# Optimization experiments

Hardware: AMD Instinct MI355X
Metric: run time of the kernel (lower is better)

## Reference

```python
import jax, jax.numpy as jnp
import numpy as np

N_RAYS = 65536
N_SAMPLES = 2_097_152
HID = 64
L_PTS, L_DIR = 10, 4
STEP = 5e-3
WHITE_BKGD = True


def posenc(x, L):
    # x [..., 3] -> [..., 3 + 6L]
    freqs = (2.0 ** jnp.arange(L)).astype(x.dtype)            # [L]
    ang = x[..., None, :] * freqs[:, None]                     # [..., L, 3]
    enc = jnp.concatenate([jnp.sin(ang), jnp.cos(ang)], -1)   # [..., L, 6]
    return jnp.concatenate([x, enc.reshape(x.shape[:-1] + (6 * L,))], -1)


def setup_inputs() -> dict:
    key = jax.random.key(0)
    ks = jax.random.split(key, 12)
    rays_o = jax.random.normal(ks[0], (N_RAYS, 3), jnp.float32)
    viewdirs = jax.random.normal(ks[1], (N_RAYS, 3), jnp.float32)
    viewdirs = viewdirs / jnp.linalg.norm(viewdirs, axis=-1, keepdims=True)
    ray_indices = jnp.sort(jax.random.randint(ks[2], (N_SAMPLES,), 0, N_RAYS, jnp.int32))
    t_starts = jax.random.uniform(ks[3], (N_SAMPLES,), jnp.float32, 0.0, 4.0)
    t_ends = t_starts + STEP

    def w(k, shape):
        return jax.random.normal(k, shape, jnp.float32) / jnp.sqrt(shape[0])

    D_PTS = 3 + 6 * L_PTS   # 63
    D_DIR = 3 + 6 * L_DIR   # 27
    return dict(
        rays_o=rays_o, viewdirs=viewdirs, t_starts=t_starts, t_ends=t_ends,
        W1=w(ks[4], (D_PTS, HID)), b1=jnp.zeros((HID,), jnp.float32),
        W2=w(ks[5], (HID, HID)), b2=jnp.zeros((HID,), jnp.float32),
        Wd=w(ks[6], (HID, 1)), bd=jnp.zeros((1,), jnp.float32),
        Wf=w(ks[7], (HID, HID)), bf=jnp.zeros((HID,), jnp.float32),
        Wr1=w(ks[8], (HID + D_DIR, HID)), br1=jnp.zeros((HID,), jnp.float32),
        Wr2=w(ks[9], (HID, 3)), br2=jnp.zeros((3,), jnp.float32),
        ray_indices=ray_indices,
    )


def reference(rays_o, viewdirs, t_starts, t_ends,
              W1, b1, W2, b2, Wd, bd, Wf, bf, Wr1, br1, Wr2, br2,
              ray_indices):
    t_mid = 0.5 * (t_starts + t_ends)                     # [S]
    o = rays_o[ray_indices]                               # gather [S,3]
    d = viewdirs[ray_indices]                             # gather [S,3]
    pts = o + d * t_mid[:, None]                          # [S,3]

    # small NeRF MLP (self.net): sigma + view-dependent rgb
    h = jax.nn.relu(posenc(pts, L_PTS) @ W1 + b1)
    h = jax.nn.relu(h @ W2 + b2)
    sigma = jax.nn.relu((h @ Wd + bd)[:, 0])              # relu(density)
    feat = h @ Wf + bf
    hd = jax.nn.relu(jnp.concatenate([feat, posenc(d, L_DIR)], -1) @ Wr1 + br1)
    rgb = jax.nn.sigmoid(hd @ Wr2 + br2)                  # [S,3]

    alpha = 1.0 - jnp.exp(-sigma * (t_ends - t_starts))   # [S], in [0,1)

    # per-ray exclusive transmittance via segment exclusive cumsum in log space
    log1m = jnp.log1p(-jnp.clip(alpha, 0.0, 1.0 - 1e-7))  # <= 0
    excl = jnp.cumsum(log1m) - log1m                      # global exclusive cumsum
    counts = jax.ops.segment_sum(jnp.ones_like(ray_indices), ray_indices, N_RAYS)
    start_idx = jnp.cumsum(counts) - counts               # first sample of each ray
    offset = jnp.where(counts > 0, excl[jnp.clip(start_idx, 0, N_SAMPLES - 1)], 0.0)
    T = jnp.exp(excl - offset[ray_indices])               # transmittance [S]
    w = T * alpha                                         # render weights [S]

    colors = jax.ops.segment_sum(w[:, None] * rgb, ray_indices, N_RAYS)   # [R,3]
    opac = jax.ops.segment_sum(w, ray_indices, N_RAYS)                    # [R]
    depth = jax.ops.segment_sum(w * t_mid, ray_indices, N_RAYS)           # [R]

    bkgd = 1.0 if WHITE_BKGD else 0.0
    colors = colors + (1.0 - opac)[:, None] * bkgd
    return colors, opac[:, None], depth[:, None]
```

## Files before the change

kernel.cpp:

```cpp
#include <hip/hip_runtime.h>
#include <math.h>

#define NR 65536
#define NS 2097152

typedef __attribute__((ext_vector_type(4))) float f32x4;
typedef __attribute__((ext_vector_type(2))) float f32x2;
typedef __attribute__((ext_vector_type(8))) short short8;



__device__ __forceinline__ uint packbf(float a, float b) {
    __bf16 lo = (__bf16)a, hi = (__bf16)b;
    ushort ul = __builtin_bit_cast(ushort, lo);
    ushort uh = __builtin_bit_cast(ushort, hi);
    return (uint)ul | ((uint)uh << 16);
}
__device__ __forceinline__ float bflo(uint u) { return __builtin_bit_cast(float, u << 16); }

__global__ void setup_kernel(const float* __restrict__ viewdirs,
                             uint4* __restrict__ dtab,
                             int* __restrict__ start, int* __restrict__ end,
                             const float* __restrict__ W1, const float* __restrict__ W2,
                             const float* __restrict__ Wf, const float* __restrict__ Wr1,
                             const float* __restrict__ Wd, const float* __restrict__ Wr2,
                             uint4* __restrict__ wfrag) {
    int b = blockIdx.x, tid = threadIdx.x;
    if (b < 256) {
        int r = b * 256 + tid;
        float dx = viewdirs[3 * r + 0], dy = viewdirs[3 * r + 1], dz = viewdirs[3 * r + 2];
        float de[32];
        de[0] = dx; de[1] = dy; de[2] = dz;
        float sx = __sinf(dx), cx = __cosf(dx);
        float sy = __sinf(dy), cy = __cosf(dy);
        float sz = __sinf(dz), cz = __cosf(dz);
        #pragma unroll
        for (int l = 0; l < 4; ++l) {
            de[3 + 6 * l + 0] = sx; de[3 + 6 * l + 1] = sy; de[3 + 6 * l + 2] = sz;
            de[3 + 6 * l + 3] = cx; de[3 + 6 * l + 4] = cy; de[3 + 6 * l + 5] = cz;
            float nsx = 2.0f * sx * cx, nsy = 2.0f * sy * cy, nsz = 2.0f * sz * cz;
            cx = fmaf(-2.0f * sx, sx, 1.0f);
            cy = fmaf(-2.0f * sy, sy, 1.0f);
            cz = fmaf(-2.0f * sz, sz, 1.0f);
            sx = nsx; sy = nsy; sz = nsz;
        }
        #pragma unroll
        for (int k = 27; k < 32; ++k) de[k] = 0.0f;
        #pragma unroll
        for (int c = 0; c < 4; ++c) {
            uint4 q = make_uint4(packbf(de[8 * c + 0], de[8 * c + 1]),
                                 packbf(de[8 * c + 2], de[8 * c + 3]),
                                 packbf(de[8 * c + 4], de[8 * c + 5]),
                                 packbf(de[8 * c + 6], de[8 * c + 7]));
            dtab[(size_t)r * 4 + c] = q;
        }
    } else if (b < 512) {
        int r = (b - 256) * 256 + tid;
        start[r] = 0; end[r] = 0;
    } else {
        int t = (b - 512) * 256 + tid;
        if (t >= 40 * 64) return;
        int f = t >> 6, lane = t & 63;
        int c = lane & 15;
        uint q[4];
        if (f < 36) {
            const float* W; int kmax, fl;
            if (f < 8)       { W = W1;  kmax = 63; fl = f; }
            else if (f < 16) { W = W2;  kmax = 64; fl = f - 8; }
            else if (f < 24) { W = Wf;  kmax = 64; fl = f - 16; }
            else             { W = Wr1; kmax = 91; fl = f - 24; }
            int ks = fl >> 2, ft = fl & 3;
            int n = ft * 16 + c;
            int kb = ks * 32 + ((lane >> 4) * 8);
            #pragma unroll
            for (int j = 0; j < 4; ++j) {
                int k0 = kb + 2 * j, k1 = k0 + 1;
                float v0 = (k0 < kmax) ? W[k0 * 64 + n] : 0.0f;
                float v1 = (k1 < kmax) ? W[k1 * 64 + n] : 0.0f;
                q[j] = packbf(v0, v1);
            }
        } else if (f < 38) {
            int kb = (f - 36) * 32 + ((lane >> 4) * 8);
            #pragma unroll
            for (int j = 0; j < 4; ++j) {
                float v0 = (c == 0) ? Wd[kb + 2 * j] : 0.0f;
                float v1 = (c == 0) ? Wd[kb + 2 * j + 1] : 0.0f;
                q[j] = packbf(v0, v1);
            }
        } else {
            int kb = (f - 38) * 32 + ((lane >> 4) * 8);
            #pragma unroll
            for (int j = 0; j < 4; ++j) {
                float v0 = (c < 3) ? Wr2[(kb + 2 * j) * 3 + c] : 0.0f;
                float v1 = (c < 3) ? Wr2[(kb + 2 * j + 1) * 3 + c] : 0.0f;
                q[j] = packbf(v0, v1);
            }
        }
        wfrag[(size_t)f * 64 + lane] = make_uint4(q[0], q[1], q[2], q[3]);
    }
}

template <int KS, bool RELU, bool SIGMA, bool DIRB>
__device__ __forceinline__ void dense_layer(uint* S, const uint4* __restrict__ wfrag,
                                            int fb, const float* __restrict__ bias,
                                            float bd0, const uint (&ro)[2],
                                            const uint (&wo)[4],
                                            int lane, const uint4 (&dirB)[4],
                                            float* sigout) {
    const int g = lane >> 4;
    uint4 wf[KS * 4];
    #pragma unroll
    for (int i = 0; i < KS * 4; ++i) wf[i] = wfrag[(size_t)(fb + i) * 64 + lane];
    uint4 wsg[2];
    if constexpr (SIGMA) {
        wsg[0] = wfrag[36 * 64 + lane];
        wsg[1] = wfrag[37 * 64 + lane];
    }
    float4 bfr[4];
    #pragma unroll
    for (int ft = 0; ft < 4; ++ft)
        bfr[ft] = *(const float4*)(bias + 16 * ft + 4 * g);

    #pragma unroll
    for (int st = 0; st < 4; ++st) {
        const uint stoff = (uint)st * 512u;
        uint4 B[KS];
        #pragma unroll
        for (int ks = 0; ks < KS; ++ks) {
            if (DIRB && ks == KS - 1) B[ks] = dirB[st];
            else B[ks] = *(const uint4*)&S[ro[ks] + stoff];
        }
        f32x4 acc[4];
        #pragma unroll
        for (int ft = 0; ft < 4; ++ft)
            acc[ft] = (f32x4){bfr[ft].x, bfr[ft].y, bfr[ft].z, bfr[ft].w};
        f32x4 sacc;
        if constexpr (SIGMA) sacc = (f32x4){(g == 0) ? bd0 : 0.0f, 0.0f, 0.0f, 0.0f};
        #pragma unroll
        for (int ks = 0; ks < KS; ++ks) {
            short8 bv = __builtin_bit_cast(short8, B[ks]);
            #pragma unroll
            for (int ft = 0; ft < 4; ++ft)
                acc[ft] = __builtin_amdgcn_mfma_f32_16x16x32_bf16(
                    __builtin_bit_cast(short8, wf[ks * 4 + ft]), bv, acc[ft], 0, 0, 0);
            if constexpr (SIGMA)
                sacc = __builtin_amdgcn_mfma_f32_16x16x32_bf16(
                    __builtin_bit_cast(short8, wsg[ks]), bv, sacc, 0, 0, 0);
        }
        #pragma unroll
        for (int ft = 0; ft < 4; ++ft) {
            f32x2 lo = {acc[ft][0], acc[ft][1]};
            f32x2 hi = {acc[ft][2], acc[ft][3]};
            if constexpr (RELU) {
                lo = __builtin_elementwise_max(lo, (f32x2){0.0f, 0.0f});
                hi = __builtin_elementwise_max(hi, (f32x2){0.0f, 0.0f});
            }
            uint2 v = make_uint2(packbf(lo.x, lo.y), packbf(hi.x, hi.y));
            *(uint2*)&S[wo[ft] + stoff] = v;
        }
        if constexpr (SIGMA) sigout[st] = sacc[0];
    }
}

__global__ __launch_bounds__(256, 4) void fused_mlp(
    const float* __restrict__ rays_o, const float* __restrict__ viewdirs,
    const float* __restrict__ t_starts, const float* __restrict__ t_ends,
    const float* __restrict__ b1, const float* __restrict__ b2,
    const float* __restrict__ bd, const float* __restrict__ bf_,
    const float* __restrict__ br1, const float* __restrict__ br2,
    const int* __restrict__ ridx, const uint4* __restrict__ wfrag,
    const uint4* __restrict__ dtab, uint2* __restrict__ rgba,
    float* __restrict__ tmarr, int* __restrict__ start, int* __restrict__ end)
{
    __shared__ uint S[8192];

    const int tid = threadIdx.x;
    const int w = tid >> 6, lane = tid & 63;
    const int g = lane >> 4, s = lane & 15;
    const uint sm = (uint)(s & 7);
    const uint wgb = (uint)w * 2048u;
    const uint rowb = wgb + (uint)s * 32u;
    const int sb0 = blockIdx.x * 256 + w * 64;

    int ridx4[4];
    #pragma unroll
    for (int st = 0; st < 4; ++st) ridx4[st] = ridx[sb0 + st * 16 + s];
    uint4 dirB[4];
    #pragma unroll
    for (int st = 0; st < 4; ++st) dirB[st] = dtab[(size_t)ridx4[st] * 4 + g];

    const int si = sb0 + g * 16 + s;
    const int rr = ridx4[g];

    {
        int r_prev = ridx[(si == 0) ? 0 : si - 1];
        int r_next = ridx[(si == NS - 1) ? NS - 1 : si + 1];
        if (si == 0 || r_prev != rr) start[rr] = si;
        if (si == NS - 1 || r_next != rr) end[rr] = si + 1;
    }

    float ts = t_starts[si], te = t_ends[si];
    float tm = 0.5f * (ts + te), dtv = te - ts;
    float dx = viewdirs[3 * rr + 0], dy = viewdirs[3 * rr + 1], dz = viewdirs[3 * rr + 2];
    float px = rays_o[3 * rr + 0] + dx * tm;
    float py = rays_o[3 * rr + 1] + dy * tm;
    float pz = rays_o[3 * rr + 2] + dz * tm;
    tmarr[si] = tm;

    const uint ownbase = wgb + (uint)g * 512u + (uint)s * 32u;
    uint ro[2], wo[4];
    #pragma unroll
    for (int ks = 0; ks < 2; ++ks)
        ro[ks] = rowb + 4u * (((uint)(g + 4 * ks)) ^ sm);
    #pragma unroll
    for (int ft = 0; ft < 4; ++ft)
        wo[ft] = rowb + 4u * (((uint)(2 * ft + (g >> 1))) ^ sm) + 2u * (uint)(g & 1);

    {
        float enc[64];
        enc[0] = px; enc[1] = py; enc[2] = pz;
        f32x2 sxy = {__sinf(px), __sinf(py)};
        f32x2 cxy = {__cosf(px), __cosf(py)};
        float sz = __sinf(pz), cz = __cosf(pz);
        #pragma unroll
        for (int l = 0; l < 10; ++l) {
            enc[3 + 6 * l + 0] = sxy.x; enc[3 + 6 * l + 1] = sxy.y; enc[3 + 6 * l + 2] = sz;
            enc[3 + 6 * l + 3] = cxy.x; enc[3 + 6 * l + 4] = cxy.y; enc[3 + 6 * l + 5] = cz;
            f32x2 nsxy = 2.0f * sxy * cxy;
            cxy = 1.0f - 2.0f * sxy * sxy;
            float nsz = 2.0f * sz * cz;
            cz = fmaf(-2.0f * sz, sz, 1.0f);
            sxy = nsxy; sz = nsz;
        }
        enc[63] = 0.0f;
        #pragma unroll
        for (int ch = 0; ch < 8; ++ch) {
            uint4 q = make_uint4(packbf(enc[8 * ch + 0], enc[8 * ch + 1]),
                                 packbf(enc[8 * ch + 2], enc[8 * ch + 3]),
                                 packbf(enc[8 * ch + 4], enc[8 * ch + 5]),
                                 packbf(enc[8 * ch + 6], enc[8 * ch + 7]));
            *(uint4*)&S[ownbase + 4u * (((uint)ch) ^ sm)] = q;
        }
    }

    float sig4[4];
    float bd0 = bd[0];
    uint4 dummy[4];

    dense_layer<2, true,  false, false>(S, wfrag,  0, b1,  0.0f, ro, wo, lane, dummy, sig4);
    dense_layer<2, true,  false, false>(S, wfrag,  8, b2,  0.0f, ro, wo, lane, dummy, sig4);
    dense_layer<2, false, true,  false>(S, wfrag, 16, bf_, bd0,  ro, wo, lane, dummy, sig4);
    dense_layer<3, true,  false, true >(S, wfrag, 24, br1, 0.0f, ro, wo, lane, dirB, sig4);

    {
        uint4 wr0 = wfrag[38 * 64 + lane], wr1f = wfrag[39 * 64 + lane];
        float c0 = br2[0], c1 = br2[1], c2 = br2[2];
        #pragma unroll
        for (int st = 0; st < 4; ++st) {
            const uint stoff = (uint)st * 512u;
            uint4 B0 = *(const uint4*)&S[ro[0] + stoff];
            uint4 B1 = *(const uint4*)&S[ro[1] + stoff];
            f32x4 acc = (g == 0) ? (f32x4){c0, c1, c2, 0.0f}
                                 : (f32x4){0.0f, 0.0f, 0.0f, 0.0f};
            acc = __builtin_amdgcn_mfma_f32_16x16x32_bf16(
                __builtin_bit_cast(short8, wr0), __builtin_bit_cast(short8, B0), acc, 0, 0, 0);
            acc = __builtin_amdgcn_mfma_f32_16x16x32_bf16(
                __builtin_bit_cast(short8, wr1f), __builtin_bit_cast(short8, B1), acc, 0, 0, 0);
            float dte = __shfl(dtv, st * 16 + (lane & 15));
            if (lane < 16) {
                float sg = fmaxf(sig4[st], 0.0f);
                float alpha = 1.0f - __expf(-sg * dte);
                float r0 = 1.0f / (1.0f + __expf(-acc[0]));
                float r1 = 1.0f / (1.0f + __expf(-acc[1]));
                float r2 = 1.0f / (1.0f + __expf(-acc[2]));
                uint2 o;
                o.x = packbf(r0, r1);
                o.y = packbf(r2, alpha);
                rgba[sb0 + st * 16 + lane] = o;
            }
        }
    }
}

__global__ void render_kernel(const uint2* __restrict__ rgba,
                              const float* __restrict__ tmarr,
                              const int* __restrict__ start,
                              const int* __restrict__ end,
                              float* __restrict__ out)
{
    int r = blockIdx.x * blockDim.x + threadIdx.x;
    if (r >= NR) return;
    int sb = start[r], e = end[r];
    float T = 1.0f, c0 = 0.0f, c1 = 0.0f, c2 = 0.0f, op = 0.0f, dp = 0.0f;
    for (int i = sb; i < e; ++i) {
        uint2 q = rgba[i];
        float tmid = tmarr[i];
        float vr = bflo(q.x & 0xffffu), vg = bflo(q.x >> 16);
        float vb = bflo(q.y & 0xffffu), va = bflo(q.y >> 16);
        float wgt = T * va;
        c0 += wgt * vr; c1 += wgt * vg; c2 += wgt * vb;
        op += wgt; dp += wgt * tmid;
        T *= (1.0f - va);
    }
    float bg = 1.0f - op;
    c0 += bg; c1 += bg; c2 += bg;
    out[3 * r + 0] = c0;
    out[3 * r + 1] = c1;
    out[3 * r + 2] = c2;
    out[3 * NR + r] = op;
    out[4 * NR + r] = dp;
}

extern "C" void kernel_launch(void* const* d_in, const int* in_sizes, int n_in,
                              void* d_out, int out_size, void* d_ws, size_t ws_size,
                              hipStream_t stream) {
    const float* rays_o   = (const float*)d_in[0];
    const float* viewdirs = (const float*)d_in[1];
    const float* t_starts = (const float*)d_in[2];
    const float* t_ends   = (const float*)d_in[3];
    const float* W1  = (const float*)d_in[4];
    const float* b1  = (const float*)d_in[5];
    const float* W2  = (const float*)d_in[6];
    const float* b2  = (const float*)d_in[7];
    const float* Wd  = (const float*)d_in[8];
    const float* bd  = (const float*)d_in[9];
    const float* Wf  = (const float*)d_in[10];
    const float* bf_ = (const float*)d_in[11];
    const float* Wr1 = (const float*)d_in[12];
    const float* br1 = (const float*)d_in[13];
    const float* Wr2 = (const float*)d_in[14];
    const float* br2 = (const float*)d_in[15];
    const int* ridx  = (const int*)d_in[16];
    float* out = (float*)d_out;

    char* ws = (char*)d_ws;
    uint2* rgba  = (uint2*)ws;
    float* tmarr = (float*)(ws + (size_t)NS * 8);
    int* start   = (int*)(ws + (size_t)NS * 12);
    int* end     = start + NR;
    uint4* wfrag = (uint4*)(ws + (size_t)NS * 12 + (size_t)NR * 8);
    uint4* dtab  = (uint4*)(ws + (size_t)NS * 12 + (size_t)NR * 8 + 40 * 64 * 16);

    setup_kernel<<<522, 256, 0, stream>>>(viewdirs, dtab, start, end,
                                          W1, W2, Wf, Wr1, Wd, Wr2, wfrag);
    fused_mlp<<<NS / 256, 256, 0, stream>>>(
        rays_o, viewdirs, t_starts, t_ends,
        b1, b2, bd, bf_, br1, br2, ridx, wfrag, dtab, rgba, tmarr, start, end);
    render_kernel<<<NR / 256, 256, 0, stream>>>(rgba, tmarr, start, end, out);
}
```

Measured before the change: 143.0 us.

## Double-buffer MLP weight fragments in registers and prefetch next layer

Weight fragments for each dense layer are now loaded into one of two register buffers one layer ahead, so global loads for layer k+1 overlap the MFMA work of layer k. The first two layers' weights are loaded at kernel start, before the gathers and positional encoding. Launch bounds drop from 4 to 3 blocks per SM to leave room for the extra 24 uint4 registers per thread, which lowers occupancy and latency hiding from other waves.

```diff
diff --git a/kernel.cpp b/kernel.cpp
--- a/kernel.cpp
+++ b/kernel.cpp
@@ -100,22 +100,21 @@
     }
 }
 
+template <int N>
+__device__ __forceinline__ void loadf(uint4* dst, const uint4* __restrict__ wfrag,
+                                      int fb, int lane) {
+    #pragma unroll
+    for (int i = 0; i < N; ++i) dst[i] = wfrag[(size_t)(fb + i) * 64 + lane];
+}
+
 template <int KS, bool RELU, bool SIGMA, bool DIRB>
-__device__ __forceinline__ void dense_layer(uint* S, const uint4* __restrict__ wfrag,
-                                            int fb, const float* __restrict__ bias,
+__device__ __forceinline__ void dense_layer(uint* S, const uint4 (&wf)[12],
+                                            const float* __restrict__ bias,
                                             float bd0, const uint (&ro)[2],
                                             const uint (&wo)[4],
                                             int lane, const uint4 (&dirB)[4],
                                             float* sigout) {
     const int g = lane >> 4;
-    uint4 wf[KS * 4];
-    #pragma unroll
-    for (int i = 0; i < KS * 4; ++i) wf[i] = wfrag[(size_t)(fb + i) * 64 + lane];
-    uint4 wsg[2];
-    if constexpr (SIGMA) {
-        wsg[0] = wfrag[36 * 64 + lane];
-        wsg[1] = wfrag[37 * 64 + lane];
-    }
     float4 bfr[4];
     #pragma unroll
     for (int ft = 0; ft < 4; ++ft)
@@ -145,7 +144,7 @@
                     __builtin_bit_cast(short8, wf[ks * 4 + ft]), bv, acc[ft], 0, 0, 0);
             if constexpr (SIGMA)
                 sacc = __builtin_amdgcn_mfma_f32_16x16x32_bf16(
-                    __builtin_bit_cast(short8, wsg[ks]), bv, sacc, 0, 0, 0);
+                    __builtin_bit_cast(short8, wf[8 + ks]), bv, sacc, 0, 0, 0);
         }
         #pragma unroll
         for (int ft = 0; ft < 4; ++ft) {
@@ -162,7 +161,7 @@
     }
 }
 
-__global__ __launch_bounds__(256, 4) void fused_mlp(
+__global__ __launch_bounds__(256, 3) void fused_mlp(
     const float* __restrict__ rays_o, const float* __restrict__ viewdirs,
     const float* __restrict__ t_starts, const float* __restrict__ t_ends,
     const float* __restrict__ b1, const float* __restrict__ b2,
@@ -182,6 +181,10 @@
     const uint rowb = wgb + (uint)s * 32u;
     const int sb0 = blockIdx.x * 256 + w * 64;
 
+    uint4 wfA[12], wfB[12];
+    loadf<8>(wfA, wfrag, 0, lane);
+    loadf<8>(wfB, wfrag, 8, lane);
+
     int ridx4[4];
     #pragma unroll
     for (int st = 0; st < 4; ++st) ridx4[st] = ridx[sb0 + st * 16 + s];
@@ -247,13 +250,21 @@
     float bd0 = bd[0];
     uint4 dummy[4];
 
-    dense_layer<2, true,  false, false>(S, wfrag,  0, b1,  0.0f, ro, wo, lane, dummy, sig4);
-    dense_layer<2, true,  false, false>(S, wfrag,  8, b2,  0.0f, ro, wo, lane, dummy, sig4);
-    dense_layer<2, false, true,  false>(S, wfrag, 16, bf_, bd0,  ro, wo, lane, dummy, sig4);
-    dense_layer<3, true,  false, true >(S, wfrag, 24, br1, 0.0f, ro, wo, lane, dirB, sig4);
+    dense_layer<2, true,  false, false>(S, wfA, b1,  0.0f, ro, wo, lane, dummy, sig4);
+    loadf<8>(wfA, wfrag, 16, lane);
+    wfA[8] = wfrag[36 * 64 + lane];
+    wfA[9] = wfrag[37 * 64 + lane];
+
+    dense_layer<2, true,  false, false>(S, wfB, b2,  0.0f, ro, wo, lane, dummy, sig4);
+    loadf<12>(wfB, wfrag, 24, lane);
+
+    dense_layer<2, false, true,  false>(S, wfA, bf_, bd0,  ro, wo, lane, dummy, sig4);
+    uint4 wr0 = wfrag[38 * 64 + lane];
+    uint4 wr1f = wfrag[39 * 64 + lane];
+
+    dense_layer<3, true,  false, true >(S, wfB, br1, 0.0f, ro, wo, lane, dirB, sig4);
 
     {
-        uint4 wr0 = wfrag[38 * 64 + lane], wr1f = wfrag[39 * 64 + lane];
         float c0 = br2[0], c1 = br2[1], c2 = br2[2];
         #pragma unroll
         for (int st = 0; st < 4; ++st) {
```

Measured after the change: 156.5 us. +9.4%, slower.

## Fold linear feature layer into first rendering layer weights and bias

Applied to the files above, without the earlier changes.

Because the feature layer has no activation, its weight matrix is premultiplied into the first 64 rows of the rendering layer in the setup kernel, and the combined bias is precomputed. The fused MLP then runs one combined layer that also produces sigma, removing a full dense layer with its MFMAs and LDS round trip per sample. The precomputed product is rounded to bf16 once, which changes numerics slightly.

```diff
diff --git a/kernel.cpp b/kernel.cpp
--- a/kernel.cpp
+++ b/kernel.cpp
@@ -24,7 +24,8 @@
                              const float* __restrict__ W1, const float* __restrict__ W2,
                              const float* __restrict__ Wf, const float* __restrict__ Wr1,
                              const float* __restrict__ Wd, const float* __restrict__ Wr2,
-                             uint4* __restrict__ wfrag) {
+                             const float* __restrict__ bf_, const float* __restrict__ br1,
+                             uint4* __restrict__ wfrag, float* __restrict__ b34) {
     int b = blockIdx.x, tid = threadIdx.x;
     if (b < 256) {
         int r = b * 256 + tid;
@@ -57,21 +58,18 @@
     } else if (b < 512) {
         int r = (b - 256) * 256 + tid;
         start[r] = 0; end[r] = 0;
-    } else {
+    } else if (b < 520) {
         int t = (b - 512) * 256 + tid;
-        if (t >= 40 * 64) return;
         int f = t >> 6, lane = t & 63;
-        int c = lane & 15;
+        int c = lane & 15, g2 = lane >> 4;
         uint q[4];
-        if (f < 36) {
-            const float* W; int kmax, fl;
-            if (f < 8)       { W = W1;  kmax = 63; fl = f; }
-            else if (f < 16) { W = W2;  kmax = 64; fl = f - 8; }
-            else if (f < 24) { W = Wf;  kmax = 64; fl = f - 16; }
-            else             { W = Wr1; kmax = 91; fl = f - 24; }
+        if (f < 16) {
+            const float* W = (f < 8) ? W1 : W2;
+            int kmax = (f < 8) ? 63 : 64;
+            int fl = f & 7;
             int ks = fl >> 2, ft = fl & 3;
             int n = ft * 16 + c;
-            int kb = ks * 32 + ((lane >> 4) * 8);
+            int kb = ks * 32 + g2 * 8;
             #pragma unroll
             for (int j = 0; j < 4; ++j) {
                 int k0 = kb + 2 * j, k1 = k0 + 1;
@@ -79,8 +77,34 @@
                 float v1 = (k1 < kmax) ? W[k1 * 64 + n] : 0.0f;
                 q[j] = packbf(v0, v1);
             }
-        } else if (f < 38) {
-            int kb = (f - 36) * 32 + ((lane >> 4) * 8);
+        } else if (f < 24) {
+            int fl = f - 16;
+            int ks = fl >> 2, ft = fl & 3;
+            int m = ft * 16 + c;
+            int kb = ks * 32 + g2 * 8;
+            #pragma unroll
+            for (int j = 0; j < 4; ++j) {
+                int k0 = kb + 2 * j, k1 = k0 + 1;
+                float v0 = 0.0f, v1 = 0.0f;
+                for (int p = 0; p < 64; ++p) {
+                    float w = Wr1[p * 64 + m];
+                    v0 = fmaf(Wf[k0 * 64 + p], w, v0);
+                    v1 = fmaf(Wf[k1 * 64 + p], w, v1);
+                }
+                q[j] = packbf(v0, v1);
+            }
+        } else if (f < 28) {
+            int n = (f - 24) * 16 + c;
+            int kb = 64 + g2 * 8;
+            #pragma unroll
+            for (int j = 0; j < 4; ++j) {
+                int k0 = kb + 2 * j, k1 = k0 + 1;
+                float v0 = (k0 < 91) ? Wr1[k0 * 64 + n] : 0.0f;
+                float v1 = (k1 < 91) ? Wr1[k1 * 64 + n] : 0.0f;
+                q[j] = packbf(v0, v1);
+            }
+        } else if (f < 30) {
+            int kb = (f - 28) * 32 + g2 * 8;
             #pragma unroll
             for (int j = 0; j < 4; ++j) {
                 float v0 = (c == 0) ? Wd[kb + 2 * j] : 0.0f;
@@ -88,7 +112,7 @@
                 q[j] = packbf(v0, v1);
             }
         } else {
-            int kb = (f - 38) * 32 + ((lane >> 4) * 8);
+            int kb = (f - 30) * 32 + g2 * 8;
             #pragma unroll
             for (int j = 0; j < 4; ++j) {
                 float v0 = (c < 3) ? Wr2[(kb + 2 * j) * 3 + c] : 0.0f;
@@ -97,6 +121,12 @@
             }
         }
         wfrag[(size_t)f * 64 + lane] = make_uint4(q[0], q[1], q[2], q[3]);
+    } else {
+        if (tid < 64) {
+            float acc = br1[tid];
+            for (int k = 0; k < 64; ++k) acc = fmaf(bf_[k], Wr1[k * 64 + tid], acc);
+            b34[tid] = acc;
+        }
     }
 }
 
@@ -113,8 +143,8 @@
     for (int i = 0; i < KS * 4; ++i) wf[i] = wfrag[(size_t)(fb + i) * 64 + lane];
     uint4 wsg[2];
     if constexpr (SIGMA) {
-        wsg[0] = wfrag[36 * 64 + lane];
-        wsg[1] = wfrag[37 * 64 + lane];
+        wsg[0] = wfrag[28 * 64 + lane];
+        wsg[1] = wfrag[29 * 64 + lane];
     }
     float4 bfr[4];
     #pragma unroll
@@ -143,9 +173,11 @@
             for (int ft = 0; ft < 4; ++ft)
                 acc[ft] = __builtin_amdgcn_mfma_f32_16x16x32_bf16(
                     __builtin_bit_cast(short8, wf[ks * 4 + ft]), bv, acc[ft], 0, 0, 0);
-            if constexpr (SIGMA)
-                sacc = __builtin_amdgcn_mfma_f32_16x16x32_bf16(
-                    __builtin_bit_cast(short8, wsg[ks]), bv, sacc, 0, 0, 0);
+            if constexpr (SIGMA) {
+                if (ks < 2)
+                    sacc = __builtin_amdgcn_mfma_f32_16x16x32_bf16(
+                        __builtin_bit_cast(short8, wsg[ks]), bv, sacc, 0, 0, 0);
+            }
         }
         #pragma unroll
         for (int ft = 0; ft < 4; ++ft) {
@@ -166,8 +198,8 @@
     const float* __restrict__ rays_o, const float* __restrict__ viewdirs,
     const float* __restrict__ t_starts, const float* __restrict__ t_ends,
     const float* __restrict__ b1, const float* __restrict__ b2,
-    const float* __restrict__ bd, const float* __restrict__ bf_,
-    const float* __restrict__ br1, const float* __restrict__ br2,
+    const float* __restrict__ bd, const float* __restrict__ b34,
+    const float* __restrict__ br2,
     const int* __restrict__ ridx, const uint4* __restrict__ wfrag,
     const uint4* __restrict__ dtab, uint2* __restrict__ rgba,
     float* __restrict__ tmarr, int* __restrict__ start, int* __restrict__ end)
@@ -249,11 +281,10 @@
 
     dense_layer<2, true,  false, false>(S, wfrag,  0, b1,  0.0f, ro, wo, lane, dummy, sig4);
     dense_layer<2, true,  false, false>(S, wfrag,  8, b2,  0.0f, ro, wo, lane, dummy, sig4);
-    dense_layer<2, false, true,  false>(S, wfrag, 16, bf_, bd0,  ro, wo, lane, dummy, sig4);
-    dense_layer<3, true,  false, true >(S, wfrag, 24, br1, 0.0f, ro, wo, lane, dirB, sig4);
+    dense_layer<3, true,  true,  true >(S, wfrag, 16, b34, bd0,  ro, wo, lane, dirB, sig4);
 
     {
-        uint4 wr0 = wfrag[38 * 64 + lane], wr1f = wfrag[39 * 64 + lane];
+        uint4 wr0 = wfrag[30 * 64 + lane], wr1f = wfrag[31 * 64 + lane];
         float c0 = br2[0], c1 = br2[1], c2 = br2[2];
         #pragma unroll
         for (int st = 0; st < 4; ++st) {
@@ -339,12 +370,14 @@
     int* start   = (int*)(ws + (size_t)NS * 12);
     int* end     = start + NR;
     uint4* wfrag = (uint4*)(ws + (size_t)NS * 12 + (size_t)NR * 8);
-    uint4* dtab  = (uint4*)(ws + (size_t)NS * 12 + (size_t)NR * 8 + 40 * 64 * 16);
-
-    setup_kernel<<<522, 256, 0, stream>>>(viewdirs, dtab, start, end,
-                                          W1, W2, Wf, Wr1, Wd, Wr2, wfrag);
+    float* b34   = (float*)(ws + (size_t)NS * 12 + (size_t)NR * 8 + 32 * 64 * 16);
+    uint4* dtab  = (uint4*)(ws + (size_t)NS * 12 + (size_t)NR * 8 + 32 * 64 * 16 + 256);
+
+    setup_kernel<<<521, 256, 0, stream>>>(viewdirs, dtab, start, end,
+                                          W1, W2, Wf, Wr1, Wd, Wr2, bf_, br1,
+                                          wfrag, b34);
     fused_mlp<<<NS / 256, 256, 0, stream>>>(
         rays_o, viewdirs, t_starts, t_ends,
-        b1, b2, bd, bf_, br1, br2, ridx, wfrag, dtab, rgba, tmarr, start, end);
+        b1, b2, bd, b34, br2, ridx, wfrag, dtab, rgba, tmarr, start, end);
     render_kernel<<<NR / 256, 256, 0, stream>>>(rgba, tmarr, start, end, out);
 }
```

Result: faster. 133.8 us, median of 2 (-6.5%).
